# Optimization experiments

Measured on AMD Instinct MI355X. Metric: run time of the kernel, lower is better.

## Reference

```python
import jax, jax.numpy as jnp
import numpy as np

PRE_NMS_THRESH = 0.05
PRE_NMS_TOP_N = 1000
MIN_SIZE = 0.0
TO_REMOVE = 1.0


def setup_inputs() -> dict:
    key = jax.random.key(0)
    k1, k2, k3 = jax.random.split(key, 3)
    N, C, H, W = 16, 80, 160, 160
    stride = 8.0
    # FCOS location grid: centers of stride-8 cells, (x, y) order
    xs = (jnp.arange(W, dtype=jnp.float32) + 0.5) * stride
    ys = (jnp.arange(H, dtype=jnp.float32) + 0.5) * stride
    yy, xx = jnp.meshgrid(ys, xs, indexing="ij")
    locations = jnp.stack([xx.reshape(-1), yy.reshape(-1)], axis=1)  # [L, 2]
    box_cls = jax.random.normal(k1, (N, C, H, W), dtype=jnp.float32)
    # positive l/t/r/b offsets, up to 64 px
    box_regression = jax.random.uniform(k2, (N, 4, H, W), dtype=jnp.float32) * 64.0
    centerness = jax.random.normal(k3, (N, 1, H, W), dtype=jnp.float32)
    image_sizes = jnp.full((N, 2), 1280, dtype=jnp.int32)  # (h, w) per image
    return {
        "locations": locations,
        "box_cls": box_cls,
        "box_regression": box_regression,
        "centerness": centerness,
        "image_sizes": image_sizes,
    }


def reference(locations, box_cls, box_regression, centerness, image_sizes):
    N, C, H, W = box_cls.shape
    L = H * W
    K = PRE_NMS_TOP_N
    # NCHW -> N,(H*W),C layouts, matching permute(0,2,3,1).reshape
    cls = jax.nn.sigmoid(jnp.transpose(box_cls, (0, 2, 3, 1)).reshape(N, L, C))
    reg = jnp.transpose(box_regression, (0, 2, 3, 1)).reshape(N, L, 4)
    ctr = jax.nn.sigmoid(jnp.transpose(centerness, (0, 2, 3, 1)).reshape(N, L))
    # candidate mask on raw sigmoid cls, then scores multiplied by centerness
    cand = cls > PRE_NMS_THRESH
    score = cls * ctr[:, :, None]
    # fixed-K masked top-k == (boolean filter then topk-capped) of the original
    flat = jnp.where(cand, score, -1.0).reshape(N, L * C)  # sentinel -1 < any real score
    vals, idx = jax.lax.top_k(flat, K)  # [N, K]
    loc_idx = idx // C                  # spatial location index
    labels = idx % C + 1                # classes are 1-based
    valid = vals > 0.0                  # real candidates have positive scores
    g_reg = jnp.take_along_axis(reg, loc_idx[..., None], axis=1)  # [N, K, 4]
    g_loc = locations[loc_idx]                                    # [N, K, 2]
    x1 = g_loc[..., 0] - g_reg[..., 0]
    y1 = g_loc[..., 1] - g_reg[..., 1]
    x2 = g_loc[..., 0] + g_reg[..., 2]
    y2 = g_loc[..., 1] + g_reg[..., 3]
    h = image_sizes[:, 0].astype(x1.dtype)[:, None]
    w = image_sizes[:, 1].astype(x1.dtype)[:, None]
    # clip_to_image: clamp to [0, size - TO_REMOVE]
    x1 = jnp.clip(x1, 0.0, w - TO_REMOVE)
    y1 = jnp.clip(y1, 0.0, h - TO_REMOVE)
    x2 = jnp.clip(x2, 0.0, w - TO_REMOVE)
    y2 = jnp.clip(y2, 0.0, h - TO_REMOVE)
    # remove_small_boxes via xywh widths/heights
    ws = x2 - x1 + TO_REMOVE
    hs = y2 - y1 + TO_REMOVE
    valid = valid & (ws >= MIN_SIZE) & (hs >= MIN_SIZE)
    boxes = jnp.stack([x1, y1, x2, y2], axis=-1) * valid[..., None].astype(x1.dtype)
    scores = jnp.where(valid, jnp.sqrt(jnp.maximum(vals, 0.0)), 0.0)
    return boxes, scores, labels, valid
```

## Files before the change

kernel.cpp:

```cpp
#include <hip/hip_runtime.h>
#include <math.h>

typedef unsigned int u32;
typedef unsigned long long u64;

constexpr int N_IMG = 16;
constexpr int C_CLS = 80;
constexpr int H_DIM = 160;
constexpr int W_DIM = 160;
constexpr int L_LOC = H_DIM * W_DIM;
constexpr int LC    = L_LOC * C_CLS;
constexpr int K_TOP = 1000;
constexpr int NB    = 1024;
constexpr int CAP   = 2048;
constexpr int GBUF  = 1024;
constexpr int CHUNK_L = 320;
constexpr int NSEG  = L_LOC / CHUNK_L;
constexpr int CF4   = CHUNK_L / 4;
constexpr int SPAN  = 80;
constexpr float THRESH = 0.05f;
constexpr u32 KEY_BASE = 119u << 23;
constexpr float T0     = 0.7f;
constexpr float DELTA  = 0.05f;
constexpr int B_SAFE  = ((0x3F340000u - KEY_BASE) >> 16);

constexpr size_t WS_GHIST = 0;
constexpr size_t WS_BCNT  = (size_t)N_IMG * NB * 4;
constexpr size_t WS_SPEC  = WS_BCNT + 8192;
constexpr int ZERO_WORDS  = N_IMG * NB;

__device__ inline float sigmoidf_acc(float x) { return 1.0f / (1.0f + expf(-x)); }

__device__ inline u32 score_bucket(u32 bits) {
    u32 b = (bits >= KEY_BASE) ? ((bits - KEY_BASE) >> 16) : 0u;
    return b > (u32)(NB - 1) ? (u32)(NB - 1) : b;
}

__device__ inline void bitonic_desc(u64* sk, u32 M, int tid, int nthr) {
    u32 n2 = 1024; while (n2 < M) n2 <<= 1;
    for (u32 i = tid; i < n2; i += nthr) if (i >= M) sk[i] = 0ull;
    __syncthreads();
    for (u32 k = 2; k <= n2; k <<= 1) {
        for (u32 j = k >> 1; j > 0; j >>= 1) {
            for (u32 i = tid; i < n2; i += nthr) {
                u32 ixj = i ^ j;
                if (ixj > i) {
                    u64 a = sk[i], b = sk[ixj];
                    bool front = ((i & k) == 0);
                    if (front ? (a < b) : (a > b)) { sk[i] = b; sk[ixj] = a; }
                }
            }
            __syncthreads();
        }
    }
}

__device__ inline void emit_one(int n, u64 kk, int k,
                                const float* locations, const float* breg,
                                const int* isz, float* out) {
    float* ob = out;
    float* os = out + (size_t)N_IMG * K_TOP * 4;
    float* ol = os + (size_t)N_IMG * K_TOP;
    float* ov = ol + (size_t)N_IMG * K_TOP;
    const float wimg = (float)isz[n * 2 + 1];
    const float himg = (float)isz[n * 2 + 0];
    const float* rn = breg + (size_t)n * 4 * L_LOC;
    size_t slot = (size_t)n * K_TOP + k;
    u32 vb = (u32)(kk >> 32);
    u32 idx = ~(u32)(kk & 0xFFFFFFFFull);
    float val = __uint_as_float(vb);
    int loc = (int)(idx / (u32)C_CLS);
    int c = (int)(idx - (u32)loc * (u32)C_CLS);
    float lx = locations[loc * 2 + 0], ly = locations[loc * 2 + 1];
    float r0 = rn[0 * L_LOC + loc], r1 = rn[1 * L_LOC + loc];
    float r2 = rn[2 * L_LOC + loc], r3 = rn[3 * L_LOC + loc];
    float x1 = lx - r0, y1 = ly - r1, x2 = lx + r2, y2 = ly + r3;
    x1 = fminf(fmaxf(x1, 0.0f), wimg - 1.0f);
    y1 = fminf(fmaxf(y1, 0.0f), himg - 1.0f);
    x2 = fminf(fmaxf(x2, 0.0f), wimg - 1.0f);
    y2 = fminf(fmaxf(y2, 0.0f), himg - 1.0f);
    float wsz = x2 - x1 + 1.0f, hsz = y2 - y1 + 1.0f;
    bool v = (val > 0.0f) && (wsz >= 0.0f) && (hsz >= 0.0f);
    float vf = v ? 1.0f : 0.0f;
    ob[slot * 4 + 0] = x1 * vf;
    ob[slot * 4 + 1] = y1 * vf;
    ob[slot * 4 + 2] = x2 * vf;
    ob[slot * 4 + 3] = y2 * vf;
    os[slot] = v ? sqrtf(fmaxf(val, 0.0f)) : 0.0f;
    ol[slot] = (float)(c + 1);
    ov[slot] = vf;
}

__device__ inline void emit_rows(int n, const u64* sk, u32 cand_slots, const u32* fill,
                                 const float* locations, const float* breg,
                                 const int* isz, float* out, int tid, int nthr) {
    float* ob = out;
    float* os = out + (size_t)N_IMG * K_TOP * 4;
    float* ol = os + (size_t)N_IMG * K_TOP;
    float* ov = ol + (size_t)N_IMG * K_TOP;
    for (int k = tid; k < K_TOP; k += nthr) {
        size_t slot = (size_t)n * K_TOP + k;
        if ((u32)k < cand_slots) {
            emit_one(n, sk[k], k, locations, breg, isz, out);
        } else {
            u32 fi = fill ? fill[k - (int)cand_slots] : 0u;
            ob[slot * 4 + 0] = 0.0f; ob[slot * 4 + 1] = 0.0f;
            ob[slot * 4 + 2] = 0.0f; ob[slot * 4 + 3] = 0.0f;
            os[slot] = 0.0f;
            ol[slot] = (float)((int)(fi % (u32)C_CLS) + 1);
            ov[slot] = 0.0f;
        }
    }
}

__global__ void zero_kernel(u32* __restrict__ ws32) {
    int i = blockIdx.x * blockDim.x + threadIdx.x;
    if (i < ZERO_WORDS) ws32[WS_GHIST / 4 + i] = 0u;
}

__global__ __launch_bounds__(256) void megaA_kernel(
        const float* __restrict__ cls, const float* __restrict__ ctr,
        u64* __restrict__ spec, u32* __restrict__ bcnt, u32* __restrict__ ghist) {
    __shared__ __align__(16) float xm[CHUNK_L];
    __shared__ float sct[CHUNK_L];
    __shared__ u64 sbuf[GBUF];
    __shared__ u32 lh[NB];
    __shared__ u32 lcnt, lof;
    const int tid = threadIdx.x;
    const u32 n = blockIdx.y;
    const u32 lbase = blockIdx.x * (u32)CHUNK_L;
    for (int b = tid; b < NB; b += 256) lh[b] = 0u;
    if (tid == 0) { lcnt = 0; lof = 0; }
    for (int i = tid; i < CHUNK_L; i += 256) {
        float s = sigmoidf_acc(ctr[(size_t)n * L_LOC + lbase + i]);
        sct[i] = s;
        float t = T0 / s;
        xm[i] = (t >= 1.0f) ? 3.0e38f : (logf(t / (1.0f - t)) - DELTA);
    }
    __syncthreads();
    const float* base = cls + (size_t)n * LC + lbase;
    u32 m0 = 0u, m1 = 0u, m2 = 0u, m3 = 0u;
#pragma unroll
    for (int g = 0; g < 5; ++g) {
        float4 v[5]; u32 l4a[5];
#pragma unroll
        for (int k = 0; k < 5; ++k) {
            int q = g * 5 + k;
            u32 f = (u32)q * 256u + (u32)tid;
            u32 c = f / (u32)CF4;
            u32 l4 = f - c * (u32)CF4;
            l4a[k] = l4;
            v[k] = *reinterpret_cast<const float4*>(base + (size_t)c * L_LOC + l4 * 4u);
        }
#pragma unroll
        for (int k = 0; k < 5; ++k) {
            int q = g * 5 + k;
            float4 m4 = *reinterpret_cast<const float4*>(&xm[l4a[k] * 4u]);
            u32 nib = (v[k].x >= m4.x ? 1u : 0u) | (v[k].y >= m4.y ? 2u : 0u)
                    | (v[k].z >= m4.z ? 4u : 0u) | (v[k].w >= m4.w ? 8u : 0u);
            u32 sh = (u32)(q & 7) * 4u;
            if ((q >> 3) == 0) m0 |= nib << sh;
            else if ((q >> 3) == 1) m1 |= nib << sh;
            else if ((q >> 3) == 2) m2 |= nib << sh;
            else m3 |= nib << sh;
        }
    }
    u32 words[4] = {m0, m1, m2, m3};
#pragma unroll
    for (int w = 0; w < 4; ++w) {
        u32 bits = words[w];
        while (bits) {
            u32 b = (u32)__ffs(bits) - 1u; bits &= bits - 1u;
            u32 q = (u32)w * 8u + (b >> 2), j = b & 3u;
            u32 f = q * 256u + (u32)tid;
            u32 c = f / (u32)CF4;
            u32 l4 = f - c * (u32)CF4;
            u32 li = l4 * 4u + j, loc = lbase + li;
            float x = base[(size_t)c * L_LOC + li];
            float s = sigmoidf_acc(x);
            float scr = s * sct[li];
            u32 sb = __float_as_uint(scr);
            atomicAdd(&lh[score_bucket(sb)], 1u);
            u32 p = atomicAdd(&lcnt, 1u);
            if (p < (u32)GBUF)
                sbuf[p] = ((u64)sb << 32) | (u32)(~(loc * (u32)C_CLS + c));
            else lof = 1u;
        }
    }
    __syncthreads();
    u32* hn = ghist + (size_t)n * NB;
    for (int b = tid; b < NB; b += 256) {
        u32 v = lh[b];
        if (v) atomicAdd(&hn[b], v);
    }
    const u32 m_ = lcnt > (u32)GBUF ? (u32)GBUF : lcnt;
    u64* sp = spec + ((size_t)n * NSEG + blockIdx.x) * GBUF;
    for (u32 i = tid; i < m_; i += 256) sp[i] = sbuf[i];
    if (tid == 0)
        bcnt[n * NSEG + blockIdx.x] = m_ | ((lof || lcnt > (u32)GBUF) ? 0x80000000u : 0u);
}

__global__ __launch_bounds__(1024) void finishC_kernel(
        const u32* __restrict__ ghist, const u64* __restrict__ spec,
        const u32* __restrict__ bcnt, const float* __restrict__ cls,
        const float* __restrict__ ctr, const float* __restrict__ locations,
        const float* __restrict__ breg, const int* __restrict__ isz,
        float* __restrict__ out) {
    __shared__ u32 lh[NB];
    __shared__ u64 sk[CAP];
    __shared__ u32 fill[K_TOP];
    __shared__ u32 segc[NSEG];
    __shared__ u32 sfxl[SPAN + 1];
    __shared__ u32 bkc[SPAN];
    __shared__ u32 s_b, s_cnt, s_lcnt, s_filled, s_bad;
    const int n = blockIdx.x;
    const int tid = threadIdx.x;
    const int wid = tid >> 6, lane = tid & 63;
    if (tid == 0) { s_b = 0xFFFFFFFFu; s_lcnt = 0; s_cnt = 0; s_filled = 0; s_bad = 0; }
    lh[tid] = ghist[(size_t)n * NB + tid];
    __syncthreads();
    if (tid < NSEG) {
        u32 v = bcnt[n * NSEG + tid];
        segc[tid] = v & 0x7FFFFFFFu;
        if (v & 0x80000000u) atomicOr(&s_bad, 1u);
    }
    __syncthreads();
    for (u32 off = 1; off < (u32)NB; off <<= 1) {
        u32 add = (tid + off < (u32)NB) ? lh[tid + off] : 0u;
        __syncthreads();
        lh[tid] += add;
        __syncthreads();
    }
    if (lh[tid] >= (u32)K_TOP && (tid == NB - 1 || lh[tid + 1] < (u32)K_TOP)) {
        s_b = (u32)tid; s_cnt = lh[tid];
    }
    __syncthreads();
    const u32 bstar = s_b;
    const u32 cnt_at = s_cnt;
    bool fastok = (s_bad == 0u) && (bstar != 0xFFFFFFFFu) &&
                  (bstar >= (u32)B_SAFE) && (cnt_at <= (u32)CAP);
    const u64* spn = spec + (size_t)n * NSEG * GBUF;
    if (fastok) {
        const u32 span = (u32)NB - bstar;
        const u32 keymin = KEY_BASE + (bstar << 16);
        if (tid <= (int)span) sfxl[tid] = (bstar + (u32)tid < (u32)NB) ? lh[bstar + tid] : 0u;
        if (tid < (int)span) bkc[tid] = 0u;
        __syncthreads();
        for (int sr = 0; sr < NSEG; sr += 16) {
            int s2 = sr + wid;
            u32 cnt = segc[s2];
            const u64* sp = spn + (size_t)s2 * GBUF;
            for (u32 i = lane; i < cnt; i += 64) {
                u64 e = sp[i];
                u32 bits = (u32)(e >> 32);
                if (bits >= keymin) {
                    u32 t = score_bucket(bits) - bstar;
                    u32 pos = sfxl[t + 1] + atomicAdd(&bkc[t], 1u);
                    if (pos < (u32)CAP) sk[pos] = e;
                }
            }
        }
        __syncthreads();
        for (u32 p = tid; p < cnt_at; p += 1024) {
            u64 e = sk[p];
            u32 t = score_bucket((u32)(e >> 32)) - bstar;
            u32 r = sfxl[t + 1];
            const u32 qe = sfxl[t];
            for (u32 q = sfxl[t + 1]; q < qe; ++q) r += (sk[q] > e) ? 1u : 0u;
            if (r < (u32)K_TOP)
                emit_one(n, e, (int)r, locations, breg, isz, out);
        }
        return;
    }
    lh[tid] = 0u;
    if (tid == 0) { s_b = 0xFFFFFFFFu; s_lcnt = 0; s_filled = 0; }
    __syncthreads();
    const float* cls_n = cls + (size_t)n * LC;
    const float* ctr_n = ctr + (size_t)n * L_LOC;
    for (u32 f = tid; f < (u32)LC; f += 1024) {
        float s = sigmoidf_acc(cls_n[f]);
        if (s > THRESH) {
            float scr = s * sigmoidf_acc(ctr_n[f % (u32)L_LOC]);
            atomicAdd(&lh[score_bucket(__float_as_uint(scr))], 1u);
        }
    }
    __syncthreads();
    for (u32 off = 1; off < (u32)NB; off <<= 1) {
        u32 add = (tid + off < (u32)NB) ? lh[tid + off] : 0u;
        __syncthreads();
        lh[tid] += add;
        __syncthreads();
    }
    if (lh[tid] >= (u32)K_TOP && (tid == NB - 1 || lh[tid + 1] < (u32)K_TOP))
        s_b = (u32)tid;
    __syncthreads();
    const u32 total = lh[0];
    const u32 keymin = (s_b != 0xFFFFFFFFu) ? (KEY_BASE + (s_b << 16)) : 0u;
    __syncthreads();
    for (u32 f = tid; f < (u32)LC; f += 1024) {
        float s = sigmoidf_acc(cls_n[f]);
        if (s > THRESH) {
            u32 loc = f % (u32)L_LOC;
            u32 c = f / (u32)L_LOC;
            float scr = s * sigmoidf_acc(ctr_n[loc]);
            u32 bits = __float_as_uint(scr);
            if (bits >= keymin) {
                u32 p = atomicAdd(&s_lcnt, 1u);
                if (p < (u32)CAP)
                    sk[p] = ((u64)bits << 32) | (u32)(~(loc * (u32)C_CLS + c));
            }
        }
    }
    __syncthreads();
    u32 M = s_lcnt > (u32)CAP ? (u32)CAP : s_lcnt;
    u32 cand_slots = total < (u32)K_TOP ? total : (u32)K_TOP;
    if (total < (u32)K_TOP) {
        const u32 need = (u32)K_TOP - total;
        for (u32 basei = 0; basei < (u32)LC; basei += 1024) {
            u32 idx = basei + tid;
            u32 flag = 0;
            if (idx < (u32)LC) {
                u32 loc = idx / (u32)C_CLS;
                u32 c = idx - loc * (u32)C_CLS;
                float x = cls_n[(size_t)c * L_LOC + loc];
                flag = (sigmoidf_acc(x) > THRESH) ? 0u : 1u;
            }
            lh[tid] = flag;
            __syncthreads();
            for (u32 off = 1; off < 1024; off <<= 1) {
                u32 v = (tid >= (int)off) ? lh[tid - off] : 0u;
                __syncthreads();
                lh[tid] += v;
                __syncthreads();
            }
            u32 excl = lh[tid] - flag;
            u32 pos = s_filled + excl;
            if (flag && pos < need) fill[pos] = idx;
            __syncthreads();
            if (tid == 0) s_filled += lh[1023];
            __syncthreads();
            if (s_filled >= need) break;
        }
    }
    bitonic_desc(sk, M, tid, 1024);
    emit_rows(n, sk, cand_slots, fill, locations, breg, isz, out, tid, 1024);
}

extern "C" void kernel_launch(void* const* d_in, const int* in_sizes, int n_in,
                              void* d_out, int out_size, void* d_ws, size_t ws_size,
                              hipStream_t stream) {
    const float* locations = (const float*)d_in[0];
    const float* cls       = (const float*)d_in[1];
    const float* breg      = (const float*)d_in[2];
    const float* ctr       = (const float*)d_in[3];
    const int*   isz       = (const int*)d_in[4];
    float* out = (float*)d_out;

    char* ws = (char*)d_ws;
    u32* ws32  = (u32*)ws;
    u32* ghist = (u32*)(ws + WS_GHIST);
    u32* bcnt  = (u32*)(ws + WS_BCNT);
    u64* spec  = (u64*)(ws + WS_SPEC);

    zero_kernel<<<(ZERO_WORDS + 255) / 256, 256, 0, stream>>>(ws32);
    megaA_kernel<<<dim3(NSEG, N_IMG), 256, 0, stream>>>(cls, ctr, spec, bcnt, ghist);
    finishC_kernel<<<N_IMG, 1024, 0, stream>>>(ghist, spec, bcnt, cls, ctr,
                                               locations, breg, isz, out);
}
```

Before: 60.26 us.

## Replace global histogram atomics with per-segment sparse pairs, drop zero kernel

Instead of atomically merging each block's 1024-bucket histogram into a zeroed global histogram, each block writes a compact list of (bucket, count) pairs to its own slot. The finish kernel reduces these lists into shared memory. This removes the zero-init kernel launch and the global atomic contention. In exchange the finish kernel does extra serial reduction work, and a new overflow flag sends a block down the slow path if it has more than 256 distinct non-empty buckets.

```diff
diff --git a/kernel.cpp b/kernel.cpp
--- a/kernel.cpp
+++ b/kernel.cpp
@@ -14,6 +14,7 @@
 constexpr int NB    = 1024;
 constexpr int CAP   = 2048;
 constexpr int GBUF  = 1024;
+constexpr int HPAIR = 256;
 constexpr int CHUNK_L = 320;
 constexpr int NSEG  = L_LOC / CHUNK_L;
 constexpr int CF4   = CHUNK_L / 4;
@@ -24,10 +25,10 @@
 constexpr float DELTA  = 0.05f;
 constexpr int B_SAFE  = ((0x3F340000u - KEY_BASE) >> 16);
 
-constexpr size_t WS_GHIST = 0;
-constexpr size_t WS_BCNT  = (size_t)N_IMG * NB * 4;
-constexpr size_t WS_SPEC  = WS_BCNT + 8192;
-constexpr int ZERO_WORDS  = N_IMG * NB;
+constexpr size_t WS_BCNT  = 0;
+constexpr size_t WS_HCNT  = 8192;
+constexpr size_t WS_HPAIR = 16384;
+constexpr size_t WS_SPEC  = WS_HPAIR + (size_t)N_IMG * NSEG * HPAIR * 8;
 
 __device__ inline float sigmoidf_acc(float x) { return 1.0f / (1.0f + expf(-x)); }
 
@@ -113,24 +114,20 @@
     }
 }
 
-__global__ void zero_kernel(u32* __restrict__ ws32) {
-    int i = blockIdx.x * blockDim.x + threadIdx.x;
-    if (i < ZERO_WORDS) ws32[WS_GHIST / 4 + i] = 0u;
-}
-
 __global__ __launch_bounds__(256) void megaA_kernel(
         const float* __restrict__ cls, const float* __restrict__ ctr,
-        u64* __restrict__ spec, u32* __restrict__ bcnt, u32* __restrict__ ghist) {
+        u64* __restrict__ spec, u32* __restrict__ bcnt,
+        u32* __restrict__ hcnt, u64* __restrict__ hpairs) {
     __shared__ __align__(16) float xm[CHUNK_L];
     __shared__ float sct[CHUNK_L];
     __shared__ u64 sbuf[GBUF];
     __shared__ u32 lh[NB];
-    __shared__ u32 lcnt, lof;
+    __shared__ u32 lcnt, lof, hcl;
     const int tid = threadIdx.x;
     const u32 n = blockIdx.y;
     const u32 lbase = blockIdx.x * (u32)CHUNK_L;
     for (int b = tid; b < NB; b += 256) lh[b] = 0u;
-    if (tid == 0) { lcnt = 0; lof = 0; }
+    if (tid == 0) { lcnt = 0; lof = 0; hcl = 0; }
     for (int i = tid; i < CHUNK_L; i += 256) {
         float s = sigmoidf_acc(ctr[(size_t)n * L_LOC + lbase + i]);
         sct[i] = s;
@@ -188,28 +185,38 @@
         }
     }
     __syncthreads();
-    u32* hn = ghist + (size_t)n * NB;
+    u64* hp = hpairs + ((size_t)n * NSEG + blockIdx.x) * HPAIR;
     for (int b = tid; b < NB; b += 256) {
         u32 v = lh[b];
-        if (v) atomicAdd(&hn[b], v);
-    }
+        if (v) {
+            u32 p = atomicAdd(&hcl, 1u);
+            if (p < (u32)HPAIR) hp[p] = ((u64)(u32)b << 32) | v;
+            else lof = 1u;
+        }
+    }
+    __syncthreads();
     const u32 m_ = lcnt > (u32)GBUF ? (u32)GBUF : lcnt;
     u64* sp = spec + ((size_t)n * NSEG + blockIdx.x) * GBUF;
     for (u32 i = tid; i < m_; i += 256) sp[i] = sbuf[i];
-    if (tid == 0)
-        bcnt[n * NSEG + blockIdx.x] = m_ | ((lof || lcnt > (u32)GBUF) ? 0x80000000u : 0u);
+    if (tid == 0) {
+        u32 hc = hcl > (u32)HPAIR ? (u32)HPAIR : hcl;
+        hcnt[n * NSEG + blockIdx.x] = hc;
+        bcnt[n * NSEG + blockIdx.x] =
+            m_ | ((lof || lcnt > (u32)GBUF || hcl > (u32)HPAIR) ? 0x80000000u : 0u);
+    }
 }
 
 __global__ __launch_bounds__(1024) void finishC_kernel(
-        const u32* __restrict__ ghist, const u64* __restrict__ spec,
-        const u32* __restrict__ bcnt, const float* __restrict__ cls,
-        const float* __restrict__ ctr, const float* __restrict__ locations,
-        const float* __restrict__ breg, const int* __restrict__ isz,
-        float* __restrict__ out) {
+        const u64* __restrict__ hpairs, const u32* __restrict__ hcnt,
+        const u64* __restrict__ spec, const u32* __restrict__ bcnt,
+        const float* __restrict__ cls, const float* __restrict__ ctr,
+        const float* __restrict__ locations, const float* __restrict__ breg,
+        const int* __restrict__ isz, float* __restrict__ out) {
     __shared__ u32 lh[NB];
     __shared__ u64 sk[CAP];
     __shared__ u32 fill[K_TOP];
     __shared__ u32 segc[NSEG];
+    __shared__ u32 hcl[NSEG];
     __shared__ u32 sfxl[SPAN + 1];
     __shared__ u32 bkc[SPAN];
     __shared__ u32 s_b, s_cnt, s_lcnt, s_filled, s_bad;
@@ -217,12 +224,24 @@
     const int tid = threadIdx.x;
     const int wid = tid >> 6, lane = tid & 63;
     if (tid == 0) { s_b = 0xFFFFFFFFu; s_lcnt = 0; s_cnt = 0; s_filled = 0; s_bad = 0; }
-    lh[tid] = ghist[(size_t)n * NB + tid];
+    lh[tid] = 0u;
     __syncthreads();
     if (tid < NSEG) {
         u32 v = bcnt[n * NSEG + tid];
         segc[tid] = v & 0x7FFFFFFFu;
+        hcl[tid] = hcnt[n * NSEG + tid];
         if (v & 0x80000000u) atomicOr(&s_bad, 1u);
+    }
+    __syncthreads();
+    const u64* hpn = hpairs + (size_t)n * NSEG * HPAIR;
+    for (int sr = 0; sr < NSEG; sr += 16) {
+        int s2 = sr + wid;
+        u32 hc = hcl[s2];
+        const u64* hp = hpn + (size_t)s2 * HPAIR;
+        for (u32 i = lane; i < hc; i += 64) {
+            u64 pr = hp[i];
+            atomicAdd(&lh[(u32)(pr >> 32)], (u32)pr);
+        }
     }
     __syncthreads();
     for (u32 off = 1; off < (u32)NB; off <<= 1) {
@@ -357,13 +376,12 @@
     float* out = (float*)d_out;
 
     char* ws = (char*)d_ws;
-    u32* ws32  = (u32*)ws;
-    u32* ghist = (u32*)(ws + WS_GHIST);
-    u32* bcnt  = (u32*)(ws + WS_BCNT);
-    u64* spec  = (u64*)(ws + WS_SPEC);
-
-    zero_kernel<<<(ZERO_WORDS + 255) / 256, 256, 0, stream>>>(ws32);
-    megaA_kernel<<<dim3(NSEG, N_IMG), 256, 0, stream>>>(cls, ctr, spec, bcnt, ghist);
-    finishC_kernel<<<N_IMG, 1024, 0, stream>>>(ghist, spec, bcnt, cls, ctr,
+    u32* bcnt   = (u32*)(ws + WS_BCNT);
+    u32* hcnt   = (u32*)(ws + WS_HCNT);
+    u64* hpairs = (u64*)(ws + WS_HPAIR);
+    u64* spec   = (u64*)(ws + WS_SPEC);
+
+    megaA_kernel<<<dim3(NSEG, N_IMG), 256, 0, stream>>>(cls, ctr, spec, bcnt, hcnt, hpairs);
+    finishC_kernel<<<N_IMG, 1024, 0, stream>>>(hpairs, hcnt, spec, bcnt, cls, ctr,
                                                locations, breg, isz, out);
 }
```

Result: faster. 56.63 us, median of 2 (-6.0%).
